# Optimization experiments

Measured on AMD Instinct MI355X. Metric: run time of the kernel, lower is better.

Reference implementation:

```python
import jax, jax.numpy as jnp
import numpy as np

DIM = 1024
N_HEADS = 16
HEAD_DIM = DIM // N_HEADS
COND_DIM = 1024
MLP_RATIO = 4
B, S = 4, 1024
LN_EPS = 1e-5


def _layer_norm(x, w):
    # F.layer_norm without affine bias, then * weight (per original LayerNorm)
    x32 = x.astype(jnp.float32)
    mu = jnp.mean(x32, axis=-1, keepdims=True)
    var = jnp.var(x32, axis=-1, keepdims=True)
    return (x32 - mu) * jax.lax.rsqrt(var + LN_EPS) * w


def _rope(t, cos, sin):
    # t: [b, s, h, d]; cos/sin: [s, d/2]; rotate-half convention
    d2 = t.shape[-1] // 2
    t1, t2 = t[..., :d2], t[..., d2:]
    c = cos[None, :, None, :]
    s = sin[None, :, None, :]
    return jnp.concatenate([t1 * c - t2 * s, t2 * c + t1 * s], axis=-1)


def setup_inputs() -> dict:
    key = jax.random.key(0)
    ks = jax.random.split(key, 12)
    inv_freq = 1.0 / (10000.0 ** (np.arange(0, HEAD_DIM, 2) / HEAD_DIM))
    ang = np.arange(S)[:, None] * inv_freq[None, :]
    return {
        "x": jax.random.normal(ks[0], (B, S, DIM), jnp.float32),
        "cos": jnp.asarray(np.cos(ang), jnp.float32),
        "sin": jnp.asarray(np.sin(ang), jnp.float32),
        "c": jax.random.normal(ks[1], (B, COND_DIM), jnp.float32),
        "w_ln1": jnp.ones((DIM,), jnp.float32),
        "w_ln2": jnp.ones((DIM,), jnp.float32),
        "w_qkv": jax.random.normal(ks[2], (DIM, 3 * DIM), jnp.float32) * 0.02,
        "w_attn_out": jax.random.normal(ks[3], (DIM, DIM), jnp.float32) * 0.02,
        "w_mlp1": jax.random.normal(ks[4], (DIM, MLP_RATIO * DIM), jnp.float32) * 0.02,
        "b_mlp1": jnp.zeros((MLP_RATIO * DIM,), jnp.float32),
        "w_mlp2": jax.random.normal(ks[5], (MLP_RATIO * DIM, DIM), jnp.float32) * 0.02,
        "b_mlp2": jnp.zeros((DIM,), jnp.float32),
        "w_ada": jax.random.normal(ks[6], (COND_DIM, 6 * DIM), jnp.float32) * 0.02,
        "b_ada": jax.random.normal(ks[7], (6 * DIM,), jnp.float32) * 0.02,
    }


def reference(x, cos, sin, c, w_ln1, w_ln2, w_qkv, w_attn_out,
              w_mlp1, b_mlp1, w_mlp2, b_mlp2, w_ada, b_ada):
    b, s, dim = x.shape
    # adaLN modulation: [b, 6*dim] -> six [b, 1, dim] chunks
    mod = (c @ w_ada + b_ada)[:, None, :]
    shift_msa, scale_msa, gate_msa, shift_mlp, scale_mlp, gate_mlp = jnp.split(mod, 6, axis=2)

    x_skip = x
    h = _layer_norm(x, w_ln1) * (1.0 + scale_msa) + shift_msa
    qkv = (h @ w_qkv).reshape(b, s, 3, N_HEADS, HEAD_DIM)
    q = _rope(qkv[:, :, 0], cos, sin)
    k = _rope(qkv[:, :, 1], cos, sin)
    v = qkv[:, :, 2]

    scale = 1.0 / jnp.sqrt(jnp.asarray(HEAD_DIM, x.dtype))
    scores = jnp.einsum('bshd,bthd->bhst', q, k) * scale  # [b,h,s,s]
    attn = jax.nn.softmax(scores, axis=-1)
    o = jnp.einsum('bhst,bthd->bshd', attn, v).reshape(b, s, dim)

    x = x_skip + gate_msa * (o @ w_attn_out)

    h2 = _layer_norm(x, w_ln2) * (1.0 + scale_mlp) + shift_mlp
    m = jax.nn.gelu(h2 @ w_mlp1 + b_mlp1, approximate=True) @ w_mlp2 + b_mlp2
    return x + gate_mlp * m
```

## Files before the change

### kernel.cpp

```cpp
#include <hip/hip_runtime.h>
#include <stdint.h>

typedef unsigned short u16;
typedef __bf16 bf16x8 __attribute__((ext_vector_type(8)));
typedef float f32x4 __attribute__((ext_vector_type(4)));

#define MOD6  6144

__device__ __forceinline__ float b2f(unsigned int u) {
    union { unsigned int i; float f; } z; z.i = u << 16; return z.f;
}
__device__ __forceinline__ u16 f2b(float f) {
    union { float f; unsigned int i; } z; z.f = f;
    unsigned int i = z.i;
    return (u16)((i + 0x7fffu + ((i >> 16) & 1u)) >> 16);
}
union U4 { uint4 u; u16 s[8]; };
union U2 { uint2 u; u16 s[4]; };
union B8 { bf16x8 v; unsigned int w[4]; };

__device__ __forceinline__ float ldf(const void* p, size_t i, int isbf) {
    if (isbf) return b2f(((const u16*)p)[i]);
    return ((const float*)p)[i];
}
__device__ __forceinline__ void load4(const void* p, size_t i, int isbf, float* v) {
    if (isbf) {
        U2 t; t.u = *(const uint2*)((const u16*)p + i);
#pragma unroll
        for (int e = 0; e < 4; e++) v[e] = b2f(t.s[e]);
    } else {
        float4 f = *(const float4*)((const float*)p + i);
        v[0] = f.x; v[1] = f.y; v[2] = f.z; v[3] = f.w;
    }
}

__device__ __forceinline__ void gld16(u16* lds, const u16* g) {
    __builtin_amdgcn_global_load_lds(
        (__attribute__((address_space(1))) void*)(g),
        (__attribute__((address_space(3))) void*)(lds), 16, 0, 0);
}

__global__ void detect_dtype(const unsigned int* __restrict__ w, int* __restrict__ flag) {
    if (threadIdx.x == 0 && blockIdx.x == 0)
        *flag = (w[0] == 0x3F803F80u) ? 1 : 0;
}

__global__ void transpose_any(const void* __restrict__ in, u16* __restrict__ out,
                              int K, int N, const int* __restrict__ flag) {
    const int isbf = *flag;
    __shared__ u16 tile[64][66];
    const int ntn = N >> 6;
    const int k0 = (blockIdx.x / ntn) << 6;
    const int n0 = (blockIdx.x % ntn) << 6;
    const int tid = threadIdx.x;
    const int r = tid >> 3;
    const int c = (tid & 7) * 8;
#pragma unroll
    for (int rr = 0; rr < 64; rr += 32) {
        const size_t base = (size_t)(k0 + r + rr) * N + n0 + c;
        u16* t = &tile[r + rr][c];
        if (isbf) {
            U4 v; v.u = *(const uint4*)((const u16*)in + base);
#pragma unroll
            for (int e = 0; e < 8; e++) t[e] = v.s[e];
        } else {
            float4 a = *(const float4*)((const float*)in + base);
            float4 b = *(const float4*)((const float*)in + base + 4);
            t[0] = f2b(a.x); t[1] = f2b(a.y); t[2] = f2b(a.z); t[3] = f2b(a.w);
            t[4] = f2b(b.x); t[5] = f2b(b.y); t[6] = f2b(b.z); t[7] = f2b(b.w);
        }
    }
    __syncthreads();
#pragma unroll
    for (int rr = 0; rr < 64; rr += 32) {
        U4 v;
#pragma unroll
        for (int e = 0; e < 8; e++) v.s[e] = tile[c + e][r + rr];
        *(uint4*)&out[(size_t)(n0 + r + rr) * K + k0 + c] = v.u;
    }
}

__global__ void ada_partial(const void* __restrict__ c, const void* __restrict__ w_ada,
                            float* __restrict__ part, const int* __restrict__ flag) {
    const int isbf = *flag;
    const int g = blockIdx.x * 256 + threadIdx.x;
    const int slice = g / 24576;
    const int idx = g - slice * 24576;
    const int b = idx / MOD6, n = idx - (idx / MOD6) * MOD6;
    const int k0 = slice * 128;
    float acc = 0.f;
    if (isbf) {
        const u16* cr = (const u16*)c + b * 1024 + k0;
        const u16* wp = (const u16*)w_ada + (size_t)k0 * MOD6 + n;
#pragma unroll 8
        for (int k = 0; k < 128; k++)
            acc += b2f(cr[k]) * b2f(wp[(size_t)k * MOD6]);
    } else {
        const float* cr = (const float*)c + b * 1024 + k0;
        const float* wp = (const float*)w_ada + (size_t)k0 * MOD6 + n;
#pragma unroll 8
        for (int k = 0; k < 128; k++)
            acc += cr[k] * wp[(size_t)k * MOD6];
    }
    part[g] = acc;
}
__global__ void ada_reduce(const float* __restrict__ part, const void* __restrict__ b_ada,
                           float* __restrict__ mod, const int* __restrict__ flag) {
    const int g = blockIdx.x * 256 + threadIdx.x;
    float acc = ldf(b_ada, g % MOD6, *flag);
#pragma unroll
    for (int s = 0; s < 8; s++) acc += part[s * 24576 + g];
    mod[g] = acc;
}

__global__ void ln_mod_kernel(const void* __restrict__ x, const void* __restrict__ w,
                              const float* __restrict__ mod, int shift_off,
                              int scale_off, u16* __restrict__ out,
                              const int* __restrict__ flag, int x_is_f32) {
    const int isbf = *flag;
    const int xb = x_is_f32 ? 0 : isbf;
    const int tk = blockIdx.x;
    const int b = tk >> 10;
    const int tid = threadIdx.x;
    float v[4];
    load4(x, (size_t)tk * 1024 + tid * 4, xb, v);
    float s = v[0] + v[1] + v[2] + v[3];
    float ss = v[0]*v[0] + v[1]*v[1] + v[2]*v[2] + v[3]*v[3];
#pragma unroll
    for (int off = 1; off < 64; off <<= 1) {
        s  += __shfl_xor(s, off);
        ss += __shfl_xor(ss, off);
    }
    __shared__ float ls[4], lss[4];
    if ((tid & 63) == 0) { ls[tid >> 6] = s; lss[tid >> 6] = ss; }
    __syncthreads();
    s  = ls[0] + ls[1] + ls[2] + ls[3];
    ss = lss[0] + lss[1] + lss[2] + lss[3];
    const float mu  = s * (1.f / 1024.f);
    const float var = ss * (1.f / 1024.f) - mu * mu;
    const float rstd = rsqrtf(var + 1e-5f);
    float wv[4];
    load4(w, (size_t)tid * 4, isbf, wv);
    const float* mb = mod + (size_t)b * MOD6;
    U2 o;
#pragma unroll
    for (int e = 0; e < 4; e++) {
        const int col = tid * 4 + e;
        float n = (v[e] - mu) * rstd * wv[e];
        o.s[e] = f2b(n * (1.f + mb[scale_off + col]) + mb[shift_off + col]);
    }
    *(uint2*)(out + (size_t)tk * 1024 + tid * 4) = o.u;
}

__global__ void out_init(const float* __restrict__ res, const float* __restrict__ gate,
                         const void* __restrict__ bias, float* __restrict__ out,
                         const int* __restrict__ flag) {
    const int isbf = *flag;
    const int g = blockIdx.x * 256 + threadIdx.x;
    const int col = (g & 255) * 4;
    const int row = g >> 8;
    const int b = row >> 10;
    float bv[4];
    load4(bias, (size_t)col, isbf, bv);
    const float* gp = gate + (size_t)b * MOD6 + col;
    float4 r = *(const float4*)(res + (size_t)row * 1024 + col);
    float4 o;
    o.x = r.x + gp[0] * bv[0];
    o.y = r.y + gp[1] * bv[1];
    o.z = r.z + gp[2] * bv[2];
    o.w = r.w + gp[3] * bv[3];
    *(float4*)(out + (size_t)row * 1024 + col) = o;
}

#define EPI_STORE 0
#define EPI_RES_GATE 1
#define EPI_GELU_BIAS 2
#define EPI_ATOMIC_GATE 4

template <int EPI>
__launch_bounds__(256, 2)
__global__ void gemm128_bt(const u16* __restrict__ A, const u16* __restrict__ Bt,
                           void* __restrict__ Cv, int M, int N, int K,
                           const void* __restrict__ res, const float* __restrict__ gate,
                           const void* __restrict__ bias, const int* __restrict__ flag,
                           int Ks) {
    __shared__ __align__(16) u16 sA[2][128 * 32];
    __shared__ __align__(16) u16 sB[2][128 * 32];
    const int isbf = flag ? *flag : 0;
    const int tid = threadIdx.x;
    const int lane = tid & 63;
    const int w = tid >> 6;
    const int wm = w >> 1, wn = w & 1;
    const int c16 = lane & 15, quad = lane >> 4;

    int bx, by, bz;
    {
        const int nx = gridDim.x, ny = gridDim.y, nz = gridDim.z;
        const int flat = blockIdx.x + nx * (blockIdx.y + ny * blockIdx.z);
        const int q = flat & 7;
        const int s = flat >> 3;
        const int g = s / nx;
        bx = s - g * nx;
        const int p = q * ((ny * nz) >> 3) + g;
        by = p % ny;
        bz = p / ny;
    }
    const int m0 = by * 128, n0 = bx * 128;
    const int kt0 = bz * Ks;

    const int srow = lane >> 2;
    const int schunk = lane & 3;
    const int gchunk = schunk ^ (srow & 3);

    const u16* gA = A + (size_t)m0 * K + 8 * gchunk + kt0;
    const u16* gB = Bt + (size_t)n0 * K + 8 * gchunk + kt0;
    const int cs = quad ^ (c16 & 3);

    const int r0 = 16 * w + srow;
    const int r1 = r0 + 64;
    const int d0 = r0 * 32 + 8 * schunk;
    const int d1 = r1 * 32 + 8 * schunk;

    f32x4 acc[4][4];
#pragma unroll
    for (int i = 0; i < 4; i++)
#pragma unroll
        for (int j = 0; j < 4; j++) acc[i][j] = (f32x4){0.f, 0.f, 0.f, 0.f};

    gld16(&sA[0][d0], gA + (size_t)r0 * K);
    gld16(&sB[0][d0], gB + (size_t)r0 * K);
    gld16(&sA[0][d1], gA + (size_t)r1 * K);
    gld16(&sB[0][d1], gB + (size_t)r1 * K);
    __syncthreads();

    const int nt = Ks >> 5;
    int cur = 0;
#pragma unroll 1
    for (int t = 0; t < nt; ++t) {
        if (t + 1 < nt) {
            const int kt = (t + 1) << 5;
            u16* dA = &sA[cur ^ 1][0];
            u16* dB = &sB[cur ^ 1][0];
            gld16(dA + d0, gA + (size_t)r0 * K + kt);
            gld16(dB + d0, gB + (size_t)r0 * K + kt);
            gld16(dA + d1, gA + (size_t)r1 * K + kt);
            gld16(dB + d1, gB + (size_t)r1 * K + kt);
        }
        const u16* fA = &sA[cur][0];
        const u16* fB = &sB[cur][0];
        bf16x8 af[4], bfr[4];
#pragma unroll
        for (int i = 0; i < 4; i++)
            af[i] = *(const bf16x8*)&fA[(64 * wm + 16 * i + c16) * 32 + 8 * cs];
#pragma unroll
        for (int j = 0; j < 4; j++)
            bfr[j] = *(const bf16x8*)&fB[(64 * wn + 16 * j + c16) * 32 + 8 * cs];
#pragma unroll
        for (int i = 0; i < 4; i++)
#pragma unroll
            for (int j = 0; j < 4; j++)
                acc[i][j] = __builtin_amdgcn_mfma_f32_16x16x32_bf16(
                    af[i], bfr[j], acc[i][j], 0, 0, 0);
        __syncthreads();
        cur ^= 1;
    }

#pragma unroll
    for (int i = 0; i < 4; i++) {
#pragma unroll
        for (int r = 0; r < 4; r++) {
            const int row = m0 + 64 * wm + 16 * i + 4 * quad + r;
            const int b = row >> 10;
#pragma unroll
            for (int j = 0; j < 4; j++) {
                const int col = n0 + 64 * wn + 16 * j + c16;
                float v = acc[i][j][r];
                if constexpr (EPI == EPI_GELU_BIAS) {
                    v += ldf(bias, col, isbf);
                    const float u = 0.7978845608f * (v + 0.044715f * v * v * v);
                    const float e = __expf(2.f * u);
                    const float t = 1.f - 2.f / (e + 1.f);
                    v = 0.5f * v * (1.f + t);
                } else if constexpr (EPI == EPI_RES_GATE) {
                    v = ldf(res, (size_t)row * N + col, isbf)
                        + gate[(size_t)b * MOD6 + col] * v;
                }
                if constexpr (EPI == EPI_ATOMIC_GATE) {
                    atomicAdd((float*)Cv + (size_t)row * N + col,
                              gate[(size_t)b * MOD6 + col] * v);
                } else if constexpr (EPI == EPI_RES_GATE) {
                    ((float*)Cv)[(size_t)row * N + col] = v;
                } else {
                    ((u16*)Cv)[(size_t)row * N + col] = f2b(v);
                }
            }
        }
    }
}

template <int EPI>
__launch_bounds__(512, 2)
__global__ void gemm256_bt(const u16* __restrict__ A, const u16* __restrict__ Bt,
                           void* __restrict__ Cv, int M, int N, int K,
                           const void* __restrict__ res, const float* __restrict__ gate,
                           const void* __restrict__ bias, const int* __restrict__ flag,
                           int Ks) {
    __shared__ __align__(16) u16 sA[2][256 * 32];
    __shared__ __align__(16) u16 sB[2][256 * 32];
    const int isbf = flag ? *flag : 0;
    const int tid = threadIdx.x;
    const int lane = tid & 63;
    const int w = tid >> 6;
    const int wm = w >> 2, wn = w & 3;
    const int c16 = lane & 15, quad = lane >> 4;

    int bx, by, bz;
    {
        const int nx = gridDim.x, ny = gridDim.y, nz = gridDim.z;
        const int flat = blockIdx.x + nx * (blockIdx.y + ny * blockIdx.z);
        const int q = flat & 7;
        const int s = flat >> 3;
        const int g = s / nx;
        bx = s - g * nx;
        const int p = q * ((ny * nz) >> 3) + g;
        by = p % ny;
        bz = p / ny;
    }
    const int m0 = by * 256, n0 = bx * 256;
    const int kt0 = bz * Ks;

    const int srow = tid >> 2;
    const int schunk = tid & 3;
    const int gchunk = schunk ^ (srow & 3);

    const u16* gA = A + (size_t)m0 * K + 8 * gchunk + kt0;
    const u16* gB = Bt + (size_t)n0 * K + 8 * gchunk + kt0;
    const int cs = quad ^ (c16 & 3);

    const int r0 = srow;
    const int r1 = srow + 128;
    const int d0 = r0 * 32 + 8 * schunk;
    const int d1 = r1 * 32 + 8 * schunk;

    f32x4 acc[8][4];
#pragma unroll
    for (int i = 0; i < 8; i++)
#pragma unroll
        for (int j = 0; j < 4; j++) acc[i][j] = (f32x4){0.f, 0.f, 0.f, 0.f};

    gld16(&sA[0][d0], gA + (size_t)r0 * K);
    gld16(&sA[0][d1], gA + (size_t)r1 * K);
    gld16(&sB[0][d0], gB + (size_t)r0 * K);
    gld16(&sB[0][d1], gB + (size_t)r1 * K);
    __syncthreads();

    const int nt = Ks >> 5;
    int cur = 0;
#pragma unroll 1
    for (int t = 0; t < nt; ++t) {
        if (t + 1 < nt) {
            const int kt = (t + 1) << 5;
            u16* dA = &sA[cur ^ 1][0];
            u16* dB = &sB[cur ^ 1][0];
            gld16(dA + d0, gA + (size_t)r0 * K + kt);
            gld16(dA + d1, gA + (size_t)r1 * K + kt);
            gld16(dB + d0, gB + (size_t)r0 * K + kt);
            gld16(dB + d1, gB + (size_t)r1 * K + kt);
        }
        const u16* fA = &sA[cur][0];
        const u16* fB = &sB[cur][0];
        bf16x8 af[8], bfr[4];
#pragma unroll
        for (int i = 0; i < 8; i++)
            af[i] = *(const bf16x8*)&fA[(128 * wm + 16 * i + c16) * 32 + 8 * cs];
#pragma unroll
        for (int j = 0; j < 4; j++)
            bfr[j] = *(const bf16x8*)&fB[(64 * wn + 16 * j + c16) * 32 + 8 * cs];
#pragma unroll
        for (int i = 0; i < 8; i++)
#pragma unroll
            for (int j = 0; j < 4; j++)
                acc[i][j] = __builtin_amdgcn_mfma_f32_16x16x32_bf16(
                    af[i], bfr[j], acc[i][j], 0, 0, 0);
        __syncthreads();
        cur ^= 1;
    }

#pragma unroll
    for (int i = 0; i < 8; i++) {
#pragma unroll
        for (int r = 0; r < 4; r++) {
            const int row = m0 + 128 * wm + 16 * i + 4 * quad + r;
            const int b = row >> 10;
#pragma unroll
            for (int j = 0; j < 4; j++) {
                const int col = n0 + 64 * wn + 16 * j + c16;
                float v = acc[i][j][r];
                if constexpr (EPI == EPI_GELU_BIAS) {
                    v += ldf(bias, col, isbf);
                    const float u = 0.7978845608f * (v + 0.044715f * v * v * v);
                    const float e = __expf(2.f * u);
                    const float t = 1.f - 2.f / (e + 1.f);
                    v = 0.5f * v * (1.f + t);
                }
                if constexpr (EPI == EPI_ATOMIC_GATE) {
                    atomicAdd((float*)Cv + (size_t)row * N + col,
                              gate[(size_t)b * MOD6 + col] * v);
                } else {
                    ((u16*)Cv)[(size_t)row * N + col] = f2b(v);
                }
            }
        }
    }
}

__global__ void rope_kernel(u16* __restrict__ qkv, const void* __restrict__ cosb,
                            const void* __restrict__ sinb, const int* __restrict__ flag) {
    const int isbf = *flag;
    const int g = blockIdx.x * 256 + threadIdx.x;
    const int q8 = g & 7;
    const int h = (g >> 3) & 15;
    const int tk = g >> 7;
    const int s = tk & 1023;
    const int d = q8 * 4;
    u16* row = qkv + (size_t)tk * 3072;

    float c4[4], s4[4];
    load4(cosb, (size_t)s * 32 + d, isbf, c4);
    load4(sinb, (size_t)s * 32 + d, isbf, s4);

#pragma unroll
    for (int which = 0; which < 2; which++) {
        u16* p1 = row + which * 1024 + h * 64 + d;
        u16* p2 = p1 + 32;
        U2 t1, t2;
        t1.u = *(const uint2*)p1;
        t2.u = *(const uint2*)p2;
        U2 o1, o2;
#pragma unroll
        for (int e = 0; e < 4; e++) {
            const float a = b2f(t1.s[e]), bb = b2f(t2.s[e]);
            o1.s[e] = f2b(a * c4[e] - bb * s4[e]);
            o2.s[e] = f2b(bb * c4[e] + a * s4[e]);
        }
        *(uint2*)p1 = o1.u;
        *(uint2*)p2 = o2.u;
    }
}

__launch_bounds__(256, 4)
__global__ void attn_mfma(const u16* __restrict__ qkv, u16* __restrict__ o_out) {
    __shared__ __align__(16) u16 sK[64 * 72];
    __shared__ __align__(16) u16 sVt[64 * 72];
    const int flat = blockIdx.x;
    const int xq = flat & 7, xs = flat >> 3;
    const int qt = xs & 15;
    const int bh = xq * 8 + (xs >> 4);
    const int b = bh >> 4, h = bh & 15;
    const int tid = threadIdx.x;
    const int w = tid >> 6;
    const int lane = tid & 63;
    const int c = lane & 15;
    const int quad = lane >> 4;

    const int q0 = qt * 64 + w * 16;
    bf16x8 qf0, qf1;
    {
        const u16* qrow = qkv + (size_t)(b * 1024 + q0 + c) * 3072 + h * 64;
        qf0 = *(const bf16x8*)(qrow + quad * 8);
        qf1 = *(const bf16x8*)(qrow + 32 + quad * 8);
    }
    f32x4 of[4];
#pragma unroll
    for (int dt = 0; dt < 4; dt++) of[dt] = (f32x4){0.f, 0.f, 0.f, 0.f};
    float mI = -1e30f, lI = 0.f;

    const int skey = tid >> 3;
    const int sch  = tid & 7;
    const int src0 = (((2 * quad) & 3) << 4) + c;
    const int src1 = (((2 * quad + 1) & 3) << 4) + c;

#pragma unroll 1
    for (int kt = 0; kt < 1024; kt += 64) {
        __syncthreads();
#pragma unroll
        for (int p = 0; p < 2; p++) {
            const int key = skey + p * 32;
            const u16* krow = qkv + (size_t)(b * 1024 + kt + key) * 3072 + 1024
                              + h * 64 + sch * 8;
            uint4 kv = *(const uint4*)krow;
            *(uint4*)&sK[key * 72 + sch * 8] = kv;
            U4 vv; vv.u = *(const uint4*)(krow + 1024);
#pragma unroll
            for (int e = 0; e < 8; e++) sVt[(sch * 8 + e) * 72 + key] = vv.s[e];
        }
        __syncthreads();
#pragma unroll
        for (int ks = 0; ks < 64; ks += 32) {
            bf16x8 k00 = *(const bf16x8*)&sK[(ks + c) * 72 + quad * 8];
            bf16x8 k01 = *(const bf16x8*)&sK[(ks + c) * 72 + 32 + quad * 8];
            bf16x8 k10 = *(const bf16x8*)&sK[(ks + 16 + c) * 72 + quad * 8];
            bf16x8 k11 = *(const bf16x8*)&sK[(ks + 16 + c) * 72 + 32 + quad * 8];
            f32x4 s0 = (f32x4){0.f, 0.f, 0.f, 0.f};
            f32x4 s1 = (f32x4){0.f, 0.f, 0.f, 0.f};
            s0 = __builtin_amdgcn_mfma_f32_16x16x32_bf16(k00, qf0, s0, 0, 0, 0);
            s0 = __builtin_amdgcn_mfma_f32_16x16x32_bf16(k01, qf1, s0, 0, 0, 0);
            s1 = __builtin_amdgcn_mfma_f32_16x16x32_bf16(k10, qf0, s1, 0, 0, 0);
            s1 = __builtin_amdgcn_mfma_f32_16x16x32_bf16(k11, qf1, s1, 0, 0, 0);
            float sc[8];
#pragma unroll
            for (int r = 0; r < 4; r++) { sc[r] = s0[r] * 0.125f; sc[4 + r] = s1[r] * 0.125f; }
            float tm = sc[0];
#pragma unroll
            for (int j = 1; j < 8; j++) tm = fmaxf(tm, sc[j]);
            tm = fmaxf(tm, __shfl_xor(tm, 16));
            tm = fmaxf(tm, __shfl_xor(tm, 32));
            const float mNew = fmaxf(mI, tm);
            const float alpha = __expf(mI - mNew);
            float p8[8];
            float psum = 0.f;
#pragma unroll
            for (int j = 0; j < 8; j++) { p8[j] = __expf(sc[j] - mNew); psum += p8[j]; }
            psum += __shfl_xor(psum, 16);
            psum += __shfl_xor(psum, 32);
            lI = lI * alpha + psum;
            mI = mNew;
#pragma unroll
            for (int dt = 0; dt < 4; dt++) {
#pragma unroll
                for (int r = 0; r < 4; r++) of[dt][r] *= alpha;
            }
            const unsigned int a0 = (unsigned)f2b(p8[0]) | ((unsigned)f2b(p8[1]) << 16);
            const unsigned int a1 = (unsigned)f2b(p8[2]) | ((unsigned)f2b(p8[3]) << 16);
            const unsigned int b0 = (unsigned)f2b(p8[4]) | ((unsigned)f2b(p8[5]) << 16);
            const unsigned int b1 = (unsigned)f2b(p8[6]) | ((unsigned)f2b(p8[7]) << 16);
            const unsigned int xa0 = (unsigned)__shfl((int)a0, src0);
            const unsigned int xb0 = (unsigned)__shfl((int)b0, src0);
            const unsigned int xa1 = (unsigned)__shfl((int)a1, src0);
            const unsigned int xb1 = (unsigned)__shfl((int)b1, src0);
            const unsigned int ya0 = (unsigned)__shfl((int)a0, src1);
            const unsigned int yb0 = (unsigned)__shfl((int)b0, src1);
            const unsigned int ya1 = (unsigned)__shfl((int)a1, src1);
            const unsigned int yb1 = (unsigned)__shfl((int)b1, src1);
            B8 pf;
            pf.w[0] = quad < 2 ? xa0 : xb0;
            pf.w[1] = quad < 2 ? xa1 : xb1;
            pf.w[2] = quad < 2 ? ya0 : yb0;
            pf.w[3] = quad < 2 ? ya1 : yb1;
#pragma unroll
            for (int dt = 0; dt < 4; dt++) {
                bf16x8 vf = *(const bf16x8*)&sVt[(dt * 16 + c) * 72 + ks + quad * 8];
                of[dt] = __builtin_amdgcn_mfma_f32_16x16x32_bf16(vf, pf.v, of[dt], 0, 0, 0);
            }
        }
    }
    const float inv = 1.f / lI;
    const size_t orow = (size_t)(b * 1024 + q0 + c) * 1024 + h * 64;
#pragma unroll
    for (int dt = 0; dt < 4; dt++) {
        U2 pk;
#pragma unroll
        for (int r = 0; r < 4; r++) pk.s[r] = f2b(of[dt][r] * inv);
        *(uint2*)(o_out + orow + dt * 16 + quad * 4) = pk.u;
    }
}

extern "C" void kernel_launch(void* const* d_in, const int* in_sizes, int n_in,
                              void* d_out, int out_size, void* d_ws, size_t ws_size,
                              hipStream_t stream) {
    (void)in_sizes; (void)n_in; (void)out_size; (void)ws_size;
    const void* x      = d_in[0];
    const void* cosb   = d_in[1];
    const void* sinb   = d_in[2];
    const void* c      = d_in[3];
    const void* w_ln1  = d_in[4];
    const void* w_ln2  = d_in[5];
    const void* w_qkv  = d_in[6];
    const void* w_attn = d_in[7];
    const void* w_mlp1 = d_in[8];
    const void* b_mlp1 = d_in[9];
    const void* w_mlp2 = d_in[10];
    const void* b_mlp2 = d_in[11];
    const void* w_ada  = d_in[12];
    const void* b_ada  = d_in[13];
    char* ws = (char*)d_ws;

    u16*   wT_qkv  = (u16*)(ws + 0);
    u16*   wT_attn = (u16*)(ws + 6291456);
    u16*   wT_mlp1 = (u16*)(ws + 8388608);
    u16*   wT_mlp2 = (u16*)(ws + 16777216);
    float* mod     = (float*)(ws + 25165824);
    u16*   hbuf    = (u16*)(ws + 25264128);
    u16*   big     = (u16*)(ws + 33652736);
    float* x2      = (float*)(ws + 67207168);
    int*   flag    = (int*)(ws + 83984384);
    float* part    = (float*)big;

    detect_dtype<<<1, 64, 0, stream>>>((const unsigned int*)w_ln1, flag);
    transpose_any<<<dim3(16 * 48), 256, 0, stream>>>(w_qkv, wT_qkv, 1024, 3072, flag);
    transpose_any<<<dim3(16 * 16), 256, 0, stream>>>(w_attn, wT_attn, 1024, 1024, flag);
    transpose_any<<<dim3(16 * 64), 256, 0, stream>>>(w_mlp1, wT_mlp1, 1024, 4096, flag);
    transpose_any<<<dim3(64 * 16), 256, 0, stream>>>(w_mlp2, wT_mlp2, 4096, 1024, flag);
    ada_partial<<<768, 256, 0, stream>>>(c, w_ada, part, flag);
    ada_reduce<<<96, 256, 0, stream>>>(part, b_ada, mod, flag);
    ln_mod_kernel<<<4096, 256, 0, stream>>>(x, w_ln1, mod, 0, 1024, hbuf, flag, 0);
    gemm128_bt<EPI_STORE><<<dim3(24, 32), 256, 0, stream>>>(
        hbuf, wT_qkv, big, 4096, 3072, 1024, nullptr, nullptr, nullptr, flag, 1024);
    rope_kernel<<<2048, 256, 0, stream>>>(big, cosb, sinb, flag);
    attn_mfma<<<1024, 256, 0, stream>>>(big, hbuf);
    gemm128_bt<EPI_RES_GATE><<<dim3(8, 32), 256, 0, stream>>>(
        hbuf, wT_attn, x2, 4096, 1024, 1024, x, mod + 2048, nullptr, flag, 1024);
    ln_mod_kernel<<<4096, 256, 0, stream>>>(x2, w_ln2, mod, 3072, 4096, hbuf, flag, 1);
    out_init<<<4096, 256, 0, stream>>>(x2, mod + 5120, b_mlp2, (float*)d_out, flag);
    gemm128_bt<EPI_GELU_BIAS><<<dim3(32, 32), 256, 0, stream>>>(
        hbuf, wT_mlp1, big, 4096, 4096, 1024, nullptr, nullptr, b_mlp1, flag, 1024);
    gemm256_bt<EPI_ATOMIC_GATE><<<dim3(4, 16, 8), 512, 0, stream>>>(
        big, wT_mlp2, (float*)d_out, 4096, 1024, 4096, nullptr, mod + 5120, nullptr,
        flag, 512);
}
```

Measured before the change: 515.5 us.

## Use 256x128 tile GEMM for QKV, MLP1 and MLP2 with higher occupancy

Replaces the 256x256 split-K GEMM with a 256x128 tile variant (8 waves in a 4x2 layout, each computing 64x64) and raises launch bounds to 4 blocks per CU. QKV and MLP1 now use this 512-thread kernel instead of the 128-tile 256-thread kernel, and MLP2 drops split-K from 8 to 4 with narrower N tiles. The aim is fewer accumulator registers, more resident waves to hide latency, and fewer atomics on MLP2, in exchange for lower per-block operand reuse and different grid shapes.

```diff
diff --git a/kernel.cpp b/kernel.cpp
--- a/kernel.cpp
+++ b/kernel.cpp
@@ -299,19 +299,19 @@
 }
 
 template <int EPI>
-__launch_bounds__(512, 2)
-__global__ void gemm256_bt(const u16* __restrict__ A, const u16* __restrict__ Bt,
+__launch_bounds__(512, 4)
+__global__ void gemm_bm256(const u16* __restrict__ A, const u16* __restrict__ Bt,
                            void* __restrict__ Cv, int M, int N, int K,
                            const void* __restrict__ res, const float* __restrict__ gate,
                            const void* __restrict__ bias, const int* __restrict__ flag,
                            int Ks) {
     __shared__ __align__(16) u16 sA[2][256 * 32];
-    __shared__ __align__(16) u16 sB[2][256 * 32];
+    __shared__ __align__(16) u16 sB[2][128 * 32];
     const int isbf = flag ? *flag : 0;
     const int tid = threadIdx.x;
     const int lane = tid & 63;
     const int w = tid >> 6;
-    const int wm = w >> 2, wn = w & 3;
+    const int wm = w >> 1, wn = w & 1;
     const int c16 = lane & 15, quad = lane >> 4;
 
     int bx, by, bz;
@@ -326,32 +326,28 @@
         by = p % ny;
         bz = p / ny;
     }
-    const int m0 = by * 256, n0 = bx * 256;
+    const int m0 = by * 256, n0 = bx * 128;
     const int kt0 = bz * Ks;
 
-    const int srow = tid >> 2;
-    const int schunk = tid & 3;
-    const int gchunk = schunk ^ (srow & 3);
-
-    const u16* gA = A + (size_t)m0 * K + 8 * gchunk + kt0;
-    const u16* gB = Bt + (size_t)n0 * K + 8 * gchunk + kt0;
+    const int fA1 = tid + 512;
+    const int gAo0 = (tid >> 2) * K + 8 * ((tid & 3) ^ ((tid >> 2) & 3));
+    const int gAo1 = (fA1 >> 2) * K + 8 * ((fA1 & 3) ^ ((fA1 >> 2) & 3));
+    const int gBo  = gAo0;
+    const int dA0 = tid * 8, dA1 = fA1 * 8, dB = tid * 8;
+
+    const u16* gA = A + (size_t)m0 * K + kt0;
+    const u16* gB = Bt + (size_t)n0 * K + kt0;
     const int cs = quad ^ (c16 & 3);
 
-    const int r0 = srow;
-    const int r1 = srow + 128;
-    const int d0 = r0 * 32 + 8 * schunk;
-    const int d1 = r1 * 32 + 8 * schunk;
-
-    f32x4 acc[8][4];
-#pragma unroll
-    for (int i = 0; i < 8; i++)
+    f32x4 acc[4][4];
+#pragma unroll
+    for (int i = 0; i < 4; i++)
 #pragma unroll
         for (int j = 0; j < 4; j++) acc[i][j] = (f32x4){0.f, 0.f, 0.f, 0.f};
 
-    gld16(&sA[0][d0], gA + (size_t)r0 * K);
-    gld16(&sA[0][d1], gA + (size_t)r1 * K);
-    gld16(&sB[0][d0], gB + (size_t)r0 * K);
-    gld16(&sB[0][d1], gB + (size_t)r1 * K);
+    gld16(&sA[0][dA0], gA + gAo0);
+    gld16(&sA[0][dA1], gA + gAo1);
+    gld16(&sB[0][dB],  gB + gBo);
     __syncthreads();
 
     const int nt = Ks >> 5;
@@ -360,24 +356,21 @@
     for (int t = 0; t < nt; ++t) {
         if (t + 1 < nt) {
             const int kt = (t + 1) << 5;
-            u16* dA = &sA[cur ^ 1][0];
-            u16* dB = &sB[cur ^ 1][0];
-            gld16(dA + d0, gA + (size_t)r0 * K + kt);
-            gld16(dA + d1, gA + (size_t)r1 * K + kt);
-            gld16(dB + d0, gB + (size_t)r0 * K + kt);
-            gld16(dB + d1, gB + (size_t)r1 * K + kt);
+            gld16(&sA[cur ^ 1][dA0], gA + gAo0 + kt);
+            gld16(&sA[cur ^ 1][dA1], gA + gAo1 + kt);
+            gld16(&sB[cur ^ 1][dB],  gB + gBo  + kt);
         }
         const u16* fA = &sA[cur][0];
         const u16* fB = &sB[cur][0];
-        bf16x8 af[8], bfr[4];
-#pragma unroll
-        for (int i = 0; i < 8; i++)
-            af[i] = *(const bf16x8*)&fA[(128 * wm + 16 * i + c16) * 32 + 8 * cs];
+        bf16x8 af[4], bfr[4];
+#pragma unroll
+        for (int i = 0; i < 4; i++)
+            af[i] = *(const bf16x8*)&fA[(64 * wm + 16 * i + c16) * 32 + 8 * cs];
 #pragma unroll
         for (int j = 0; j < 4; j++)
             bfr[j] = *(const bf16x8*)&fB[(64 * wn + 16 * j + c16) * 32 + 8 * cs];
 #pragma unroll
-        for (int i = 0; i < 8; i++)
+        for (int i = 0; i < 4; i++)
 #pragma unroll
             for (int j = 0; j < 4; j++)
                 acc[i][j] = __builtin_amdgcn_mfma_f32_16x16x32_bf16(
@@ -387,10 +380,10 @@
     }
 
 #pragma unroll
-    for (int i = 0; i < 8; i++) {
+    for (int i = 0; i < 4; i++) {
 #pragma unroll
         for (int r = 0; r < 4; r++) {
-            const int row = m0 + 128 * wm + 16 * i + 4 * quad + r;
+            const int row = m0 + 64 * wm + 16 * i + 4 * quad + r;
             const int b = row >> 10;
 #pragma unroll
             for (int j = 0; j < 4; j++) {
@@ -604,7 +597,7 @@
     ada_partial<<<768, 256, 0, stream>>>(c, w_ada, part, flag);
     ada_reduce<<<96, 256, 0, stream>>>(part, b_ada, mod, flag);
     ln_mod_kernel<<<4096, 256, 0, stream>>>(x, w_ln1, mod, 0, 1024, hbuf, flag, 0);
-    gemm128_bt<EPI_STORE><<<dim3(24, 32), 256, 0, stream>>>(
+    gemm_bm256<EPI_STORE><<<dim3(24, 16), 512, 0, stream>>>(
         hbuf, wT_qkv, big, 4096, 3072, 1024, nullptr, nullptr, nullptr, flag, 1024);
     rope_kernel<<<2048, 256, 0, stream>>>(big, cosb, sinb, flag);
     attn_mfma<<<1024, 256, 0, stream>>>(big, hbuf);
@@ -612,9 +605,9 @@
         hbuf, wT_attn, x2, 4096, 1024, 1024, x, mod + 2048, nullptr, flag, 1024);
     ln_mod_kernel<<<4096, 256, 0, stream>>>(x2, w_ln2, mod, 3072, 4096, hbuf, flag, 1);
     out_init<<<4096, 256, 0, stream>>>(x2, mod + 5120, b_mlp2, (float*)d_out, flag);
-    gemm128_bt<EPI_GELU_BIAS><<<dim3(32, 32), 256, 0, stream>>>(
+    gemm_bm256<EPI_GELU_BIAS><<<dim3(32, 16), 512, 0, stream>>>(
         hbuf, wT_mlp1, big, 4096, 4096, 1024, nullptr, nullptr, b_mlp1, flag, 1024);
-    gemm256_bt<EPI_ATOMIC_GATE><<<dim3(4, 16, 8), 512, 0, stream>>>(
+    gemm_bm256<EPI_ATOMIC_GATE><<<dim3(8, 16, 4), 512, 0, stream>>>(
         big, wT_mlp2, (float*)d_out, 4096, 1024, 4096, nullptr, mod + 5120, nullptr,
-        flag, 512);
-}
+        flag, 1024);
+}
```

Result: faster. 463.1 us (-10.2%).
